# Optimization experiments

Measured on AMD Instinct MI355X. Metric: run time of the kernel, lower is better.

Reference implementation:

```python
import jax, jax.numpy as jnp
import numpy as np

EMBED_DIM = 256
N_HEADS = 16
DK = EMBED_DIM // N_HEADS


def setup_inputs() -> dict:
    key = jax.random.key(0)
    ks = jax.random.split(key, 7)
    B, N, D = 32, 10000, EMBED_DIM
    scale = 1.0 / np.sqrt(D)
    ctx = jax.random.normal(ks[0], (B, D), dtype=jnp.float32)
    node_emb = jax.random.normal(ks[1], (B, N, D), dtype=jnp.float32)
    feas_mask = jax.random.randint(ks[2], (B, N), 0, 2).astype(jnp.bool_)
    Wq = jax.random.normal(ks[3], (D, D), dtype=jnp.float32) * scale
    Wk = jax.random.normal(ks[4], (D, D), dtype=jnp.float32) * scale
    Wv = jax.random.normal(ks[5], (D, D), dtype=jnp.float32) * scale
    Wo = jax.random.normal(ks[6], (D, D), dtype=jnp.float32) * scale
    return {"ctx": ctx, "node_emb": node_emb, "feas_mask": feas_mask,
            "Wq": Wq, "Wk": Wk, "Wv": Wv, "Wo": Wo}


def reference(ctx, node_emb, feas_mask, Wq, Wk, Wv, Wo):
    B, N, D = node_emb.shape
    H, dk = N_HEADS, DK
    # torch nn.Linear(no bias): y = x @ W.T
    q = (ctx @ Wq.T).reshape(B, H, dk)                    # [B,H,dk]
    k = (node_emb @ Wk.T).reshape(B, N, H, dk)            # [B,N,H,dk]
    v = (node_emb @ Wv.T).reshape(B, N, H, dk)            # [B,N,H,dk]
    logits = jnp.einsum('bhd,bnhd->bhn', q, k) / jnp.sqrt(jnp.float32(dk))
    neg_inf = jnp.finfo(logits.dtype).min
    logits = jnp.where(feas_mask[:, None, :], logits, neg_inf)
    attn = jax.nn.softmax(logits, axis=-1)                # [B,H,N]
    head_ctx = jnp.einsum('bhn,bnhd->bhd', attn, v)       # [B,H,dk]
    out = head_ctx.reshape(B, D)
    return out @ Wo.T
```

## Files before the change

### kernel.cpp

```cpp
#include <hip/hip_runtime.h>
#include <math.h>

#define NB 32
#define NN 10000
#define DIM 256
#define NH 16
#define NPART 16
#define PREC2 4112
#define IDXSTRIDE 10240

typedef short short8v __attribute__((ext_vector_type(8)));
typedef float float4v __attribute__((ext_vector_type(4)));

__device__ __forceinline__ unsigned bf16rne(float f) {
    unsigned u = __float_as_uint(f);
    return (u + 0x7FFFu + ((u >> 16) & 1u)) >> 16;
}
__device__ __forceinline__ unsigned pack2(float a, float b) {
    return bf16rne(a) | (bf16rne(b) << 16);
}
__device__ __forceinline__ short8v pack8(float4 A, float4 B) {
    union { short8v s; unsigned u[4]; } r;
    r.u[0] = pack2(A.x, A.y); r.u[1] = pack2(A.z, A.w);
    r.u[2] = pack2(B.x, B.y); r.u[3] = pack2(B.z, B.w);
    return r.s;
}
#define SWB(d) ((((d) >> 1) & 7) << 4)

__global__ void prep_compact_kernel(const float* __restrict__ ctx,
                                    const float* __restrict__ Wq,
                                    const float* __restrict__ Wk,
                                    const void* __restrict__ maskp,
                                    float* __restrict__ wt,
                                    int* __restrict__ idx,
                                    int* __restrict__ cnt) {
    int bid = blockIdx.x;
    int t = threadIdx.x, lane = t & 63, w = t >> 6;

    __shared__ float ctxL[DIM];
    __shared__ float qL[64];
    __shared__ int sflag;
    __shared__ int wcnt[4];

    if (bid < 4 * NB) {
        int b = bid >> 2, iq = bid & 3;
        ctxL[t] = ctx[b * DIM + t];
        __syncthreads();

        float4 c = ((const float4*)ctxL)[lane];
        for (int i = iq * 64 + w; i < iq * 64 + 64; i += 4) {
            float4 wq = ((const float4*)(Wq + (size_t)i * DIM))[lane];
            float s = wq.x * c.x + wq.y * c.y + wq.z * c.z + wq.w * c.w;
            #pragma unroll
            for (int off = 1; off < 64; off <<= 1) s += __shfl_xor(s, off, 64);
            if (lane == 0) qL[i - iq * 64] = s;
        }
        __syncthreads();

        #pragma unroll
        for (int hh = 0; hh < 4; ++hh) {
            int h = iq * 4 + hh;
            float a = 0.f;
            #pragma unroll
            for (int j = 0; j < 16; ++j)
                a += qL[hh * 16 + j] * Wk[(size_t)(h * 16 + j) * DIM + t];
            wt[((size_t)b * NH + h) * DIM + t] = 0.25f * a;
        }
    } else {
        int b = bid - 4 * NB;
        const int* wordbase = (const int*)maskp + (size_t)b * (NN / 4);
        int bad = 0;
        for (int i = t; i < NN / 4; i += 256)
            if ((unsigned)wordbase[i] > 1u) bad = 1;
        if (t == 0) sflag = 0;
        __syncthreads();
        if (bad) sflag = 1;
        __syncthreads();
        const bool bytemask = (sflag != 0);
        const unsigned char* m8 = (const unsigned char*)maskp + (size_t)b * NN;
        const int* m32 = (const int*)maskp + (size_t)b * NN;

        int segbeg = w * (NN / 4);
        int segend = segbeg + (NN / 4);

        int c1 = 0;
        for (int base = segbeg; base < segend; base += 64) {
            int i = base + lane;
            int pred = (i < segend) ? (bytemask ? (m8[i] != 0) : (m32[i] != 0)) : 0;
            unsigned long long bal = __ballot(pred);
            c1 += __popcll(bal);
        }
        if (lane == 0) wcnt[w] = c1;
        __syncthreads();

        int run = 0;
        for (int k = 0; k < w; ++k) run += wcnt[k];

        int* ob = idx + (size_t)b * IDXSTRIDE;
        for (int base = segbeg; base < segend; base += 64) {
            int i = base + lane;
            int pred = (i < segend) ? (bytemask ? (m8[i] != 0) : (m32[i] != 0)) : 0;
            unsigned long long bal = __ballot(pred);
            int rank = __popcll(bal & ((1ull << lane) - 1ull));
            if (pred) ob[run + rank] = i;
            run += __popcll(bal);
        }
        if (t == 0) cnt[b] = wcnt[0] + wcnt[1] + wcnt[2] + wcnt[3];
    }
}

#define XTBUF(bb) (smem + (size_t)(bb) * 32768)
#define PLBUF(bb) (smem + 65536 + (size_t)(bb) * 2304)

#define STEP_A(cc) { \
    short8v af = pack8(LA##cc, LB##cc); \
    union { short8v s; unsigned short u[8]; } U; U.s = af; \
    int d0 = g * 8 + cc * 32; \
    _Pragma("unroll") \
    for (int j = 0; j < 8; ++j) \
        *(unsigned short*)(XTc + (size_t)(d0 + j) * 128 + \
                           (ln2 ^ SWB(d0 + j))) = U.u[j]; \
    acc = __builtin_amdgcn_mfma_f32_16x16x32_bf16(af, wfrag##cc, acc, 0, 0, 0); \
}

#define PHASE_A_TAIL(tb_, cur_) { \
    char* XTc = XTBUF(cur_); char* PLc = PLBUF(cur_); \
    float4v acc = (float4v){0.f, 0.f, 0.f, 0.f}; \
    STEP_A(0) STEP_A(1) STEP_A(2) STEP_A(3) \
    STEP_A(4) STEP_A(5) STEP_A(6) STEP_A(7) \
    int mb_ = (tb_) + 16 * w + 4 * g; \
    float p0 = (mb_ + 0 < n1) ? __expf(acc[0]) : 0.f; \
    float p1 = (mb_ + 1 < n1) ? __expf(acc[1]) : 0.f; \
    float p2 = (mb_ + 2 < n1) ? __expf(acc[2]) : 0.f; \
    float p3 = (mb_ + 3 < n1) ? __expf(acc[3]) : 0.f; \
    float ts = p0 + p1 + p2 + p3; \
    ts += __shfl_xor(ts, 16, 64); \
    ts += __shfl_xor(ts, 32, 64); \
    lacc += ts; \
    *(uint2*)(PLc + hq * 144 + (16 * w + 4 * g) * 2) = \
        make_uint2(pack2(p0, p1), pack2(p2, p3)); \
}

#define PHASE_B(bb) { \
    char* XTp = XTBUF(bb); char* PLp = PLBUF(bb); \
    _Pragma("unroll") \
    for (int chunk = 0; chunk < 2; ++chunk) { \
        short8v pf = *(const short8v*)(PLp + hq * 144 + chunk * 64 + g * 16); \
        int d0 = 64 * w + hq; \
        short8v xf0 = *(const short8v*)(XTp + (size_t)(d0) * 128 + \
                                        ((chunk * 64 + g * 16) ^ SWB(d0))); \
        short8v xf1 = *(const short8v*)(XTp + (size_t)(d0 + 16) * 128 + \
                                        ((chunk * 64 + g * 16) ^ SWB(d0 + 16))); \
        short8v xf2 = *(const short8v*)(XTp + (size_t)(d0 + 32) * 128 + \
                                        ((chunk * 64 + g * 16) ^ SWB(d0 + 32))); \
        short8v xf3 = *(const short8v*)(XTp + (size_t)(d0 + 48) * 128 + \
                                        ((chunk * 64 + g * 16) ^ SWB(d0 + 48))); \
        accB0 = __builtin_amdgcn_mfma_f32_16x16x32_bf16(xf0, pf, accB0, 0, 0, 0); \
        accB1 = __builtin_amdgcn_mfma_f32_16x16x32_bf16(xf1, pf, accB1, 0, 0, 0); \
        accB2 = __builtin_amdgcn_mfma_f32_16x16x32_bf16(xf2, pf, accB2, 0, 0, 0); \
        accB3 = __builtin_amdgcn_mfma_f32_16x16x32_bf16(xf3, pf, accB3, 0, 0, 0); \
    } \
}

#define LOAD_TILE(nextpos_) \
    const float* arow = nb + (size_t)ni * DIM + g * 8; \
    float4 LA0 = *(const float4*)(arow + 0),   LB0 = *(const float4*)(arow + 4); \
    float4 LA1 = *(const float4*)(arow + 32),  LB1 = *(const float4*)(arow + 36); \
    float4 LA2 = *(const float4*)(arow + 64),  LB2 = *(const float4*)(arow + 68); \
    float4 LA3 = *(const float4*)(arow + 96),  LB3 = *(const float4*)(arow + 100); \
    float4 LA4 = *(const float4*)(arow + 128), LB4 = *(const float4*)(arow + 132); \
    float4 LA5 = *(const float4*)(arow + 160), LB5 = *(const float4*)(arow + 164); \
    float4 LA6 = *(const float4*)(arow + 192), LB6 = *(const float4*)(arow + 196); \
    float4 LA7 = *(const float4*)(arow + 224), LB7 = *(const float4*)(arow + 228); \
    int ni_next = ib[nextpos_]; \
    __builtin_amdgcn_sched_group_barrier(0x20, 17, 0);

__launch_bounds__(256, 2)
__global__ void attend_kernel(const float* __restrict__ node,
                              const int* __restrict__ idx,
                              const int* __restrict__ cntarr,
                              const float* __restrict__ wt,
                              float* __restrict__ partials) {
    __shared__ __align__(16) char smem[70400];
    float* LL = (float*)(smem + 70144);

    int b = blockIdx.x / NPART;
    int part = blockIdx.x % NPART;
    int t = threadIdx.x, lane = t & 63;
    int w = __builtin_amdgcn_readfirstlane(t >> 6);
    int hq = lane & 15, g = lane >> 4;

    int cnt = cntarr[b];
    int psz = ((cnt + NPART * 64 - 1) / (NPART * 64)) * 64;
    int n0 = part * psz;
    int n1 = n0 + psz; if (n1 > cnt) n1 = cnt;

    const float* nb = node + (size_t)b * NN * DIM;
    const int* ib = idx + (size_t)b * IDXSTRIDE;

    short8v wfrag0, wfrag1, wfrag2, wfrag3, wfrag4, wfrag5, wfrag6, wfrag7;
    {
        const float* wrow = wt + ((size_t)b * NH + hq) * DIM + g * 8;
        #define WLOAD(cc) wfrag##cc = pack8(*(const float4*)(wrow + cc * 32), \
                                            *(const float4*)(wrow + cc * 32 + 4));
        WLOAD(0) WLOAD(1) WLOAD(2) WLOAD(3) WLOAD(4) WLOAD(5) WLOAD(6) WLOAD(7)
        #undef WLOAD
    }

    float4v accB0 = (float4v){0.f,0.f,0.f,0.f};
    float4v accB1 = accB0, accB2 = accB0, accB3 = accB0;
    float lacc = 0.f;
    int ln2 = (16 * w + hq) * 2;
    int lastk = 0;

    if (n0 < n1) {
        int pos = n0 + 16 * w + hq; if (pos > cnt - 1) pos = cnt - 1;
        int ni = ib[pos];
        {
            int posn = n0 + 64 + 16 * w + hq;
            if (posn > cnt - 1) posn = cnt - 1;
            LOAD_TILE(posn)
            PHASE_A_TAIL(n0, 0)
            ni = ni_next;
        }
        __syncthreads();

        for (int tb = n0 + 64; tb < n1; tb += 64) {
            int k = (tb - n0) >> 6;
            int cur = k & 1;
            int posn = tb + 64 + 16 * w + hq;
            if (posn > cnt - 1) posn = cnt - 1;
            LOAD_TILE(posn)

            PHASE_B(cur ^ 1)
            PHASE_A_TAIL(tb, cur)

            ni = ni_next;
            lastk = k;
            __syncthreads();
        }

        PHASE_B(lastk & 1)
    }

    __syncthreads();
    float* GL = (float*)smem;
    #pragma unroll
    for (int r = 0; r < 4; ++r) {
        GL[hq * 260 + 64 * w +  0 + 4 * g + r] = accB0[r];
        GL[hq * 260 + 64 * w + 16 + 4 * g + r] = accB1[r];
        GL[hq * 260 + 64 * w + 32 + 4 * g + r] = accB2[r];
        GL[hq * 260 + 64 * w + 48 + 4 * g + r] = accB3[r];
    }
    if (lane < 16) LL[w * 16 + lane] = lacc;
    __syncthreads();

    float* rec = partials + (size_t)blockIdx.x * PREC2;
    if (t < NH) rec[t] = LL[t] + LL[16 + t] + LL[32 + t] + LL[48 + t];
    for (int i = t; i < NH * DIM; i += 256)
        rec[16 + i] = GL[(i >> 8) * 260 + (i & 255)];
}

__global__ void reduce_hc_kernel(const float* __restrict__ partials,
                                 const float* __restrict__ Wv,
                                 float* __restrict__ hcws) {
    int b = blockIdx.x >> 4, h = blockIdx.x & 15;
    int t = threadIdx.x;
    __shared__ float grow[DIM];
    __shared__ float lp[NPART];
    __shared__ float lsum;

    const float* pb = partials + (size_t)b * NPART * PREC2;
    float a = 0.f;
    for (int p = 0; p < NPART; ++p) a += pb[(size_t)p * PREC2 + 16 + h * DIM + t];
    grow[t] = a;
    if (t < NPART) lp[t] = pb[(size_t)t * PREC2 + h];
    __syncthreads();
    if (t == 0) {
        float s = 0.f;
        #pragma unroll
        for (int p = 0; p < NPART; ++p) s += lp[p];
        lsum = s;
    }
    __syncthreads();

    int i = h * 16 + (t >> 4), sub = t & 15;
    const float4* wrow = (const float4*)(Wv + (size_t)i * DIM + sub * 16);
    const float4* gr = (const float4*)(grow + sub * 16);
    float s = 0.f;
    #pragma unroll
    for (int k = 0; k < 4; ++k) {
        float4 wv = wrow[k], gv = gr[k];
        s += wv.x * gv.x + wv.y * gv.y + wv.z * gv.z + wv.w * gv.w;
    }
    s += __shfl_xor(s, 1, 64);
    s += __shfl_xor(s, 2, 64);
    s += __shfl_xor(s, 4, 64);
    s += __shfl_xor(s, 8, 64);
    if (sub == 0) hcws[(size_t)b * DIM + i] = s / lsum;
}

__global__ void out_kernel(const float* __restrict__ hcws,
                           const float* __restrict__ Wo,
                           float* __restrict__ out) {
    int b = blockIdx.x >> 3, o = blockIdx.x & 7;
    int t = threadIdx.x;
    int e = o * 32 + (t >> 3), sub = t & 7;
    const float4* wrow = (const float4*)(Wo + (size_t)e * DIM + sub * 32);
    const float4* hrow = (const float4*)(hcws + (size_t)b * DIM + sub * 32);
    float a = 0.f;
    #pragma unroll
    for (int k = 0; k < 8; ++k) {
        float4 wv = wrow[k], hv = hrow[k];
        a += wv.x * hv.x + wv.y * hv.y + wv.z * hv.z + wv.w * hv.w;
    }
    a += __shfl_xor(a, 1, 64);
    a += __shfl_xor(a, 2, 64);
    a += __shfl_xor(a, 4, 64);
    if (sub == 0) out[(size_t)b * DIM + e] = a;
}

extern "C" void kernel_launch(void* const* d_in, const int* in_sizes, int n_in,
                              void* d_out, int out_size, void* d_ws, size_t ws_size,
                              hipStream_t stream) {
    const float* ctx  = (const float*)d_in[0];
    const float* node = (const float*)d_in[1];
    const void*  mask = (const void*)d_in[2];
    const float* Wq   = (const float*)d_in[3];
    const float* Wk   = (const float*)d_in[4];
    const float* Wv   = (const float*)d_in[5];
    const float* Wo   = (const float*)d_in[6];
    float* out = (float*)d_out;

    float* wsf = (float*)d_ws;
    float* wt = wsf;
    float* hcws = wt + (size_t)NB * NH * DIM;
    int*   cnt = (int*)(hcws + (size_t)NB * DIM);
    int*   idx = cnt + 256;
    float* partials = (float*)(idx + (size_t)NB * IDXSTRIDE);

    prep_compact_kernel<<<NB * 4 + NB, 256, 0, stream>>>(ctx, Wq, Wk, mask, wt, idx, cnt);
    attend_kernel<<<NB * NPART, 256, 0, stream>>>(node, idx, cnt, wt, partials);
    reduce_hc_kernel<<<NB * 16, 256, 0, stream>>>(partials, Wv, hcws);
    out_kernel<<<NB * 8, 256, 0, stream>>>(hcws, Wo, out);
}
```

Measured before the change: 72.34 us.

## Prefetch next gathered tile across the barrier with a vmcnt-preserving sync

New measurement: 70.93 us (median of 2 runs). About the same (-1.9%).

```diff
diff --git a/kernel.cpp b/kernel.cpp
--- a/kernel.cpp
+++ b/kernel.cpp
@@ -26,6 +26,13 @@
     return r.s;
 }
 #define SWB(d) ((((d) >> 1) & 7) << 4)
+
+__device__ __forceinline__ void barrier_keep_vmcnt() {
+    __builtin_amdgcn_sched_barrier(0);
+    asm volatile("s_waitcnt lgkmcnt(0)");
+    __builtin_amdgcn_s_barrier();
+    __builtin_amdgcn_sched_barrier(0);
+}
 
 __global__ void prep_compact_kernel(const float* __restrict__ ctx,
                                     const float* __restrict__ Wq,
@@ -162,18 +169,21 @@
     } \
 }
 
-#define LOAD_TILE(nextpos_) \
+#define LOAD_TILE(nextpos_) { \
     const float* arow = nb + (size_t)ni * DIM + g * 8; \
-    float4 LA0 = *(const float4*)(arow + 0),   LB0 = *(const float4*)(arow + 4); \
-    float4 LA1 = *(const float4*)(arow + 32),  LB1 = *(const float4*)(arow + 36); \
-    float4 LA2 = *(const float4*)(arow + 64),  LB2 = *(const float4*)(arow + 68); \
-    float4 LA3 = *(const float4*)(arow + 96),  LB3 = *(const float4*)(arow + 100); \
-    float4 LA4 = *(const float4*)(arow + 128), LB4 = *(const float4*)(arow + 132); \
-    float4 LA5 = *(const float4*)(arow + 160), LB5 = *(const float4*)(arow + 164); \
-    float4 LA6 = *(const float4*)(arow + 192), LB6 = *(const float4*)(arow + 196); \
-    float4 LA7 = *(const float4*)(arow + 224), LB7 = *(const float4*)(arow + 228); \
-    int ni_next = ib[nextpos_]; \
-    __builtin_amdgcn_sched_group_barrier(0x20, 17, 0);
+    LA0 = *(const float4*)(arow + 0);   LB0 = *(const float4*)(arow + 4); \
+    LA1 = *(const float4*)(arow + 32);  LB1 = *(const float4*)(arow + 36); \
+    LA2 = *(const float4*)(arow + 64);  LB2 = *(const float4*)(arow + 68); \
+    LA3 = *(const float4*)(arow + 96);  LB3 = *(const float4*)(arow + 100); \
+    LA4 = *(const float4*)(arow + 128); LB4 = *(const float4*)(arow + 132); \
+    LA5 = *(const float4*)(arow + 160); LB5 = *(const float4*)(arow + 164); \
+    LA6 = *(const float4*)(arow + 192); LB6 = *(const float4*)(arow + 196); \
+    LA7 = *(const float4*)(arow + 224); LB7 = *(const float4*)(arow + 228); \
+    ni = ib[nextpos_]; \
+    __builtin_amdgcn_sched_group_barrier(0x20, 17, 0); \
+}
+
+#define CLAMPPOS(base_) ((base_) + 16 * w + hq > cnt - 1 ? cnt - 1 : (base_) + 16 * w + hq)
 
 __launch_bounds__(256, 2)
 __global__ void attend_kernel(const float* __restrict__ node,
@@ -211,36 +221,34 @@
     float4v accB1 = accB0, accB2 = accB0, accB3 = accB0;
     float lacc = 0.f;
     int ln2 = (16 * w + hq) * 2;
-    int lastk = 0;
+
+    float4 LA0, LA1, LA2, LA3, LA4, LA5, LA6, LA7;
+    float4 LB0, LB1, LB2, LB3, LB4, LB5, LB6, LB7;
+    int ni;
 
     if (n0 < n1) {
-        int pos = n0 + 16 * w + hq; if (pos > cnt - 1) pos = cnt - 1;
-        int ni = ib[pos];
-        {
-            int posn = n0 + 64 + 16 * w + hq;
-            if (posn > cnt - 1) posn = cnt - 1;
-            LOAD_TILE(posn)
-            PHASE_A_TAIL(n0, 0)
-            ni = ni_next;
-        }
-        __syncthreads();
+        int nt = (n1 - n0 + 63) >> 6;
+
+        ni = ib[CLAMPPOS(n0)];
+        LOAD_TILE(CLAMPPOS(n0 + 64))
+        PHASE_A_TAIL(n0, 0)
+        if (nt > 1) {
+            LOAD_TILE(CLAMPPOS(n0 + 128))
+        }
+        barrier_keep_vmcnt();
 
         for (int tb = n0 + 64; tb < n1; tb += 64) {
             int k = (tb - n0) >> 6;
             int cur = k & 1;
-            int posn = tb + 64 + 16 * w + hq;
-            if (posn > cnt - 1) posn = cnt - 1;
-            LOAD_TILE(posn)
-
             PHASE_B(cur ^ 1)
             PHASE_A_TAIL(tb, cur)
-
-            ni = ni_next;
-            lastk = k;
-            __syncthreads();
-        }
-
-        PHASE_B(lastk & 1)
+            if (tb + 64 < n1) {
+                LOAD_TILE(CLAMPPOS(tb + 128))
+            }
+            barrier_keep_vmcnt();
+        }
+
+        PHASE_B((nt - 1) & 1)
     }
 
     __syncthreads();
```
